# Optimization experiments

Hardware: AMD Instinct MI355X
Metric: run time of the kernel (lower is better)

## Reference

```python
import jax, jax.numpy as jnp
import numpy as np

N, C, H, W = 8, 128, 56, 56
CO = C // 8  # 16


def setup_inputs() -> dict:
    key = jax.random.key(0)
    k1, k2, k3, k4 = jax.random.split(key, 4)
    x = jax.random.normal(k1, (N, C, H, W), dtype=jnp.float32)
    # p_3: Conv2d(c*35 -> c//8, 1x1). The unfold channel order is (c, kh=5, kw=7),
    # so the 1x1 conv over c*35 channels is exactly a dilated 5x7 conv with
    # weight [CO, C, 5, 7] and rhs_dilation (2, 3).
    w3 = jax.random.normal(k2, (CO, C, 5, 7), dtype=jnp.float32) * 0.02
    w4 = jax.random.normal(k3, (CO, CO), dtype=jnp.float32) * 0.1
    w5 = jax.random.normal(k4, (C, CO), dtype=jnp.float32) * 0.1
    return {"x": x, "w3": w3, "w4": w4, "w5": w5}


def reference(x, w3, w4, w5):
    # Fused equivalent of: unfold(5x1, dil 2, pad 4) -> unfold(1x7, dil 3, pad 9)
    # -> 1x1 conv (c*35 -> c//8). Padding (4,4)/(9,9) keeps 'same' spatial size.
    y = jax.lax.conv_general_dilated(
        x, w3,
        window_strides=(1, 1),
        padding=((4, 4), (9, 9)),
        rhs_dilation=(2, 3),
        dimension_numbers=("NCHW", "OIHW", "NCHW"),
    )  # [N, CO, H, W]
    y = jnp.einsum("oc,nchw->nohw", w4, y)  # p_4: 1x1 conv CO->CO
    y = jnp.einsum("oc,nchw->nohw", w5, y)  # p_5: 1x1 conv CO->C
    return y
```

## Files before the change

### kernel.cpp

```cpp
#include <hip/hip_runtime.h>

#define BN 8
#define BC 128
#define BH 56
#define BW 56
#define HW 3136
#define NTAP 35
#define WS_WC 71680
#define WS_XP (WS_WC + 4096)
#define XROW 2368

typedef unsigned short u16;
typedef unsigned int u32;
typedef __bf16 bf16x8 __attribute__((ext_vector_type(8)));
typedef float f32x4 __attribute__((ext_vector_type(4)));

__device__ __forceinline__ u16 f2b(float f) {
    unsigned u = __float_as_uint(f);
    return (u16)((u + 0x7FFFu + ((u >> 16) & 1u)) >> 16);
}
__device__ __forceinline__ u32 pack2(float a, float b) {
    return (u32)f2b(a) | ((u32)f2b(b) << 16);
}
__device__ __forceinline__ void dma16(const void* g, void* l) {
    __builtin_amdgcn_global_load_lds(
        (const __attribute__((address_space(1))) u32*)g,
        (__attribute__((address_space(3))) u32*)l, 16, 0, 0);
}

__global__ __launch_bounds__(256) void prep_all(
    const float* __restrict__ x, const float* __restrict__ w3,
    const float* __restrict__ w4, const float* __restrict__ w5,
    u16* __restrict__ ws)
{
    const int b = blockIdx.x;
    const int tid = threadIdx.x;

    if (b >= 2048) {
        int i = (b - 2048) * 256 + tid;
        if (i < WS_WC) {
            int j = i & 7, lane = (i >> 3) & 63, r = i >> 9;
            int tap = r % NTAP, cc = r / NTAP;
            int q = lane >> 4, lm = lane & 15;
            ws[i] = f2b(w3[(lm * BC + cc * 32 + q * 8 + j) * NTAP + tap]);
        } else if (i < WS_WC + 4096) {
            int i2 = i - WS_WC;
            int j = i2 & 7, lane = (i2 >> 3) & 63, ot = i2 >> 9;
            int q = lane >> 4, lm = lane & 15, o = ot * 16 + lm, k = q * 8 + j;
            float s = 0.f;
            if (k < 16)
                for (int c = 0; c < 16; ++c) s += w5[o * 16 + c] * w4[c * 16 + k];
            ws[i] = f2b(s);
        }
        return;
    }

    __shared__ float ls[32][57];
    const int hp = b & 63, cc = (b >> 6) & 3, n = b >> 8;
    u32* dst = (u32*)(ws + WS_XP + (size_t)((n * 4 + cc) * 64 + hp) * XROW);
    const int gr = hp - 4;

    if ((unsigned)gr >= BH) {
        for (int i = tid; i < XROW / 2; i += 256) dst[i] = 0u;
        return;
    }
    for (int i = tid; i < 32 * 14; i += 256) {
        int c = i / 14, w4i = i % 14;
        float4 v = *(const float4*)(x + ((size_t)(n * BC + cc * 32 + c) * BH + gr) * BW + 4 * w4i);
        ls[c][4 * w4i + 0] = v.x;
        ls[c][4 * w4i + 1] = v.y;
        ls[c][4 * w4i + 2] = v.z;
        ls[c][4 * w4i + 3] = v.w;
    }
    __syncthreads();
    for (int i = tid; i < 74 * 16; i += 256) {
        int col = i >> 4, cp = i & 15;
        int gw = col - 9;
        u32 v = 0u;
        if ((unsigned)gw < BW) v = pack2(ls[2 * cp][gw], ls[2 * cp + 1][gw]);
        dst[col * 16 + cp] = v;
    }
}

__global__ __launch_bounds__(256, 4) void conv_mfma(
    const u16* __restrict__ wsT, float* __restrict__ out)
{
    __shared__ __align__(16) u16 xs[5][74][32];
    __shared__ __align__(16) u16 y3T[64][40];

    const int n = blockIdx.x & 7, h = blockIdx.x >> 3;
    const int tid = threadIdx.x, lane = tid & 63, wv = tid >> 6;
    const int q = lane >> 4, lm = lane & 15, wpos = wv * 16 + lm;

    for (int i = tid; i < 512; i += 256)
        ((u32*)&y3T[i >> 3][16])[i & 7] = 0u;

    f32x4 acc = {0.f, 0.f, 0.f, 0.f};
    char* xsf = (char*)&xs[0][0][0];
    const u16* ap = wsT + (size_t)lane * 8;

    for (int cc = 0; cc < 4; ++cc) {
        __syncthreads();

        const u16* xbase = wsT + WS_XP + (size_t)((n * 4 + cc) * 64 + h) * XROW;
        for (int k = wv; k < 24; k += 4) {
            int bb = k * 1024 + lane * 16;
            int r = bb / 4736;
            int off = bb - r * 4736;
            if (k < 23 || lane < 8)
                dma16(xbase + (size_t)(2 * r) * XROW + (off >> 1), xsf + bb);
        }
        __syncthreads();

        const u16* at = ap + (size_t)cc * NTAP * 512;
        #pragma unroll
        for (int t = 0; t < NTAP; ++t) {
            const int kh = t / 7, kw = t % 7;
            bf16x8 a = *(const bf16x8*)(at + t * 512);
            bf16x8 b = *(const bf16x8*)&xs[kh][wpos + 3 * kw][q * 8];
            acc = __builtin_amdgcn_mfma_f32_16x16x32_bf16(a, b, acc, 0, 0, 0);
        }
    }

    *(u32*)&y3T[wpos][q * 4]     = pack2(acc[0], acc[1]);
    *(u32*)&y3T[wpos][q * 4 + 2] = pack2(acc[2], acc[3]);
    __syncthreads();

    bf16x8 bfrag = *(const bf16x8*)&y3T[wpos][q * 8];
    const bool wok = (wpos < BW);
    #pragma unroll
    for (int ot = 0; ot < 8; ++ot) {
        bf16x8 afrag = *(const bf16x8*)(wsT + WS_WC + (size_t)(ot * 64 + lane) * 8);
        f32x4 c2 = {0.f, 0.f, 0.f, 0.f};
        c2 = __builtin_amdgcn_mfma_f32_16x16x32_bf16(afrag, bfrag, c2, 0, 0, 0);
        if (wok) {
            int o = ot * 16 + q * 4;
            float* po = out + ((size_t)(n * BC + o) * BH + h) * BW + wpos;
            po[0]      = c2[0];
            po[HW]     = c2[1];
            po[2 * HW] = c2[2];
            po[3 * HW] = c2[3];
        }
    }
}

extern "C" void kernel_launch(void* const* d_in, const int* in_sizes, int n_in,
                              void* d_out, int out_size, void* d_ws, size_t ws_size,
                              hipStream_t stream)
{
    (void)in_sizes; (void)n_in; (void)out_size; (void)ws_size;
    const float* x  = (const float*)d_in[0];
    const float* w3 = (const float*)d_in[1];
    const float* w4 = (const float*)d_in[2];
    const float* w5 = (const float*)d_in[3];
    u16* ws = (u16*)d_ws;

    prep_all<<<2048 + 296, 256, 0, stream>>>(x, w3, w4, w5, ws);
    conv_mfma<<<BN * BH, 256, 0, stream>>>(ws, (float*)d_out);
}
```

Baseline: 91.89 us.

## Split conv blocks by half-row and split taps across waves with LDS reduction

Each block now covers half an output row with 512 threads. The 35 taps are split across four wave groups, each group preloads its weight fragments into registers, and the partial accumulators are summed through an LDS buffer. The second-stage 1x1 output tiles are also spread across the wave groups. The aim is more waves in flight and shorter serial MFMA chains, in exchange for extra LDS traffic, an extra barrier and the input row being loaded twice (once per half-row block).

```diff
diff --git a/kernel.cpp b/kernel.cpp
--- a/kernel.cpp
+++ b/kernel.cpp
@@ -82,28 +82,35 @@
     }
 }
 
-__global__ __launch_bounds__(256, 4) void conv_mfma(
+__global__ __launch_bounds__(512, 4) void conv_mfma(
     const u16* __restrict__ wsT, float* __restrict__ out)
 {
     __shared__ __align__(16) u16 xs[5][74][32];
-    __shared__ __align__(16) u16 y3T[64][40];
+    __shared__ __align__(16) u16 y3T[32][40];
+    __shared__ __align__(16) float cbuf[2][3][64][4];
 
-    const int n = blockIdx.x & 7, h = blockIdx.x >> 3;
+    const int n = blockIdx.x & 7;
+    const int r0 = blockIdx.x >> 3;
+    const int h = r0 >> 1, wh = r0 & 1;
     const int tid = threadIdx.x, lane = tid & 63, wv = tid >> 6;
-    const int q = lane >> 4, lm = lane & 15, wpos = wv * 16 + lm;
+    const int wt = wv >> 2, g = wv & 3;
+    const int q = lane >> 4, lm = lane & 15;
+    const int wl = wt * 16 + lm;
+    const int wg = wh * 28 + wl;
+    const bool wok = (wl < 28);
 
-    for (int i = tid; i < 512; i += 256)
-        ((u32*)&y3T[i >> 3][16])[i & 7] = 0u;
+    if (tid < 256) ((u32*)&y3T[tid >> 3][16])[tid & 7] = 0u;
 
     f32x4 acc = {0.f, 0.f, 0.f, 0.f};
     char* xsf = (char*)&xs[0][0][0];
-    const u16* ap = wsT + (size_t)lane * 8;
+    const int t0 = 9 * g;
+    const int ntap = (g == 3) ? 8 : 9;
 
     for (int cc = 0; cc < 4; ++cc) {
         __syncthreads();
 
         const u16* xbase = wsT + WS_XP + (size_t)((n * 4 + cc) * 64 + h) * XROW;
-        for (int k = wv; k < 24; k += 4) {
+        for (int k = wv; k < 24; k += 8) {
             int bb = k * 1024 + lane * 16;
             int r = bb / 4736;
             int off = bb - r * 4736;
@@ -112,30 +119,57 @@
         }
         __syncthreads();
 
-        const u16* at = ap + (size_t)cc * NTAP * 512;
+        const u16* wbase = wsT + (size_t)cc * NTAP * 512 + (size_t)lane * 8;
+        bf16x8 areg[9];
         #pragma unroll
-        for (int t = 0; t < NTAP; ++t) {
-            const int kh = t / 7, kw = t % 7;
-            bf16x8 a = *(const bf16x8*)(at + t * 512);
-            bf16x8 b = *(const bf16x8*)&xs[kh][wpos + 3 * kw][q * 8];
-            acc = __builtin_amdgcn_mfma_f32_16x16x32_bf16(a, b, acc, 0, 0, 0);
+        for (int tt = 0; tt < 9; ++tt) {
+            int t = t0 + tt;
+            int tc = (t < NTAP) ? t : (NTAP - 1);
+            areg[tt] = *(const bf16x8*)(wbase + (size_t)tc * 512);
+        }
+        #pragma unroll
+        for (int tt = 0; tt < 9; ++tt) {
+            if (tt < ntap) {
+                int t = t0 + tt;
+                int kh = t / 7, kw = t - 7 * kh;
+                bf16x8 b = *(const bf16x8*)&xs[kh][wg + 3 * kw][q * 8];
+                acc = __builtin_amdgcn_mfma_f32_16x16x32_bf16(areg[tt], b, acc, 0, 0, 0);
+            }
         }
     }
 
-    *(u32*)&y3T[wpos][q * 4]     = pack2(acc[0], acc[1]);
-    *(u32*)&y3T[wpos][q * 4 + 2] = pack2(acc[2], acc[3]);
+    if (g > 0) {
+        cbuf[wt][g - 1][lane][0] = acc[0];
+        cbuf[wt][g - 1][lane][1] = acc[1];
+        cbuf[wt][g - 1][lane][2] = acc[2];
+        cbuf[wt][g - 1][lane][3] = acc[3];
+    }
+    __syncthreads();
+    if (g == 0) {
+        #pragma unroll
+        for (int p = 0; p < 3; ++p) {
+            acc[0] += cbuf[wt][p][lane][0];
+            acc[1] += cbuf[wt][p][lane][1];
+            acc[2] += cbuf[wt][p][lane][2];
+            acc[3] += cbuf[wt][p][lane][3];
+        }
+        u32 lo = wok ? pack2(acc[0], acc[1]) : 0u;
+        u32 hi = wok ? pack2(acc[2], acc[3]) : 0u;
+        *(u32*)&y3T[wl][q * 4]     = lo;
+        *(u32*)&y3T[wl][q * 4 + 2] = hi;
+    }
     __syncthreads();
 
-    bf16x8 bfrag = *(const bf16x8*)&y3T[wpos][q * 8];
-    const bool wok = (wpos < BW);
+    bf16x8 bfrag = *(const bf16x8*)&y3T[wl][q * 8];
     #pragma unroll
-    for (int ot = 0; ot < 8; ++ot) {
+    for (int i = 0; i < 2; ++i) {
+        const int ot = 2 * g + i;
         bf16x8 afrag = *(const bf16x8*)(wsT + WS_WC + (size_t)(ot * 64 + lane) * 8);
         f32x4 c2 = {0.f, 0.f, 0.f, 0.f};
         c2 = __builtin_amdgcn_mfma_f32_16x16x32_bf16(afrag, bfrag, c2, 0, 0, 0);
         if (wok) {
             int o = ot * 16 + q * 4;
-            float* po = out + ((size_t)(n * BC + o) * BH + h) * BW + wpos;
+            float* po = out + ((size_t)(n * BC + o) * BH + h) * BW + wg;
             po[0]      = c2[0];
             po[HW]     = c2[1];
             po[2 * HW] = c2[2];
@@ -156,5 +190,5 @@
     u16* ws = (u16*)d_ws;
 
     prep_all<<<2048 + 296, 256, 0, stream>>>(x, w3, w4, w5, ws);
-    conv_mfma<<<BN * BH, 256, 0, stream>>>(ws, (float*)d_out);
+    conv_mfma<<<BN * BH * 2, 512, 0, stream>>>(ws, (float*)d_out);
 }
```

After: 92.36 us. About the same (+0.5%).
